# Optimization experiments

Hardware: AMD Instinct MI355X
Metric: run time of the kernel (lower is better)

## Reference

```python
import math
import jax, jax.numpy as jnp
import numpy as np

IN_DIM = 512
OUT_DIM = 512
K = 3
EPS = 1e-8


def setup_inputs() -> dict:
    key = jax.random.key(0)
    k1, k2, k3 = jax.random.split(key, 3)
    b, h, w = 8, 64, 64
    x = jax.random.normal(k1, (b, IN_DIM, h, w), dtype=jnp.float32)
    style = jax.random.normal(k2, (b, IN_DIM), dtype=jnp.float32)
    weight = jax.random.normal(k3, (OUT_DIM, IN_DIM, K, K), dtype=jnp.float32)
    bias = jnp.zeros((OUT_DIM,), dtype=jnp.float32)
    return {"x": x, "style": style, "weight": weight, "bias": bias}


def _mod_weights(weight, style):
    # EqualizedWeight scaling: c = 1/sqrt(prod(shape[1:]))
    c = 1.0 / math.sqrt(IN_DIM * K * K)
    w = weight * c                                    # [out, in, k, k]
    ws = w[None] * (style[:, None, :, None, None] + 1.0)  # [b, out, in, k, k]
    sigma_inv = jax.lax.rsqrt(jnp.sum(ws * ws, axis=(2, 3, 4), keepdims=True) + EPS)
    return ws * sigma_inv


def reference(x, style, weight, bias):
    ws = _mod_weights(weight, style)                  # [b, out, in, k, k]

    def conv_one(xi, wi):
        # xi: [in, h, w], wi: [out, in, k, k]
        y = jax.lax.conv_general_dilated(
            xi[None], wi, window_strides=(1, 1), padding="SAME",
            dimension_numbers=("NCHW", "OIHW", "NCHW"))
        return y[0]

    out = jax.vmap(conv_one)(x, ws)                   # [b, out, h, w]
    return out + bias[None, :, None, None]
```

## Files before the change

### kernel.cpp

```cpp
#include <hip/hip_runtime.h>

#define CIN 512
#define COUT 512
#define HH 64
#define WW 64
#define BB 8
#define KTOT 4608

#define XPD 66
#define BUFSH (3 * 66 * 64)
#define ROWB (66 * 128)

typedef __attribute__((ext_vector_type(8))) short short8;
typedef __attribute__((ext_vector_type(4))) float f32x4;

__device__ inline unsigned short f2bf(float f) {
    unsigned int u = __float_as_uint(f);
    u += 0x7FFFu + ((u >> 16) & 1u);
    return (unsigned short)(u >> 16);
}

__device__ inline void gll16(const void* g, void* l) {
    __builtin_amdgcn_global_load_lds(
        (const __attribute__((address_space(1))) unsigned int*)g,
        (__attribute__((address_space(3))) unsigned int*)l, 16, 0, 0);
}

__global__ __launch_bounds__(256) void zring_kernel(unsigned short* __restrict__ xtp) {
    const int e = blockIdx.x * 256 + threadIdx.x;
    if (e >= BB * 260 * 64) return;
    const int unit = e & 63;
    const int sa = e >> 6;
    const int b = sa / 260;
    const int s = sa - b * 260;
    int yy, xx;
    if (s < 66)       { yy = 0;        xx = s; }
    else if (s < 132) { yy = 65;       xx = s - 66; }
    else if (s < 196) { yy = s - 131;  xx = 0; }
    else              { yy = s - 195;  xx = 65; }
    *(short8*)(xtp + ((size_t)(b * XPD + yy) * XPD + xx) * 512 + unit * 8) =
        (short8){0, 0, 0, 0, 0, 0, 0, 0};
}

__global__ __launch_bounds__(256) void xpose_kernel(const float* __restrict__ x,
                                                    const float* __restrict__ style,
                                                    unsigned short* __restrict__ xtp) {
    __shared__ float tile[32 * 65];
    __shared__ float sst[32];
    const int ic = blockIdx.x;
    const int y  = blockIdx.y;
    const int b  = blockIdx.z;
    const int t  = threadIdx.x;
    if (t < 32) sst[t] = style[b * CIN + ic * 32 + t] + 1.0f;
#pragma unroll
    for (int it = 0; it < 8; ++it) {
        int e = it * 256 + t;
        int ii = e >> 6, xx = e & 63;
        tile[ii * 65 + xx] = x[(((size_t)(b * CIN + ic * 32 + ii) * HH + y) << 6) + xx];
    }
    __syncthreads();
#pragma unroll
    for (int it = 0; it < 8; ++it) {
        int g = it * 256 + t;
        int xx = g >> 5, ii = g & 31;
        xtp[((size_t)(b * XPD + y + 1) * XPD + xx + 1) * 512 + ic * 32 + ii] =
            f2bf(tile[ii * 65 + xx] * sst[ii]);
    }
}

__global__ __launch_bounds__(256) void wpack_kernel(const float* __restrict__ weight,
                                                    unsigned short* __restrict__ wpk) {
    __shared__ float q[KTOT];
    const int o = blockIdx.x;
    const int t = threadIdx.x;
    const float* wrow = weight + (size_t)o * KTOT;
    const float cst = 1.0f / sqrtf((float)KTOT);
#pragma unroll
    for (int it = 0; it < 18; ++it) {
        int e = it * 256 + t;
        q[e] = wrow[e] * cst;
    }
    __syncthreads();
    const int g = o >> 4, l15 = o & 15;
    for (int m = t; m < 576; m += 256) {
        int c   = m / 36;
        int rem = m - c * 36;
        int tap = rem >> 2;
        int l4  = rem & 3;
        short8 v;
#pragma unroll
        for (int e = 0; e < 8; ++e)
            v[e] = (short)f2bf(q[(c * 32 + l4 * 8 + e) * 9 + tap]);
        *(short8*)(wpk + ((((size_t)c * 9 + tap) * 32 + g) * 64 + l4 * 16 + l15) * 8) = v;
    }
}

__global__ __launch_bounds__(256) void sigma_kernel(const float* __restrict__ weight,
                                                    const float* __restrict__ style,
                                                    float* __restrict__ siginv) {
    __shared__ float sred[4][8];
    const int o = blockIdx.x;
    const int t = threadIdx.x;
    const float* wrow = weight + (size_t)o * KTOT;
    float acc[8] = {0.f, 0.f, 0.f, 0.f, 0.f, 0.f, 0.f, 0.f};
#pragma unroll
    for (int ii = 0; ii < 2; ++ii) {
        const int i = t * 2 + ii;
        float wsq = 0.f;
#pragma unroll
        for (int tap = 0; tap < 9; ++tap) {
            float v = wrow[i * 9 + tap];
            wsq += v * v;
        }
#pragma unroll
        for (int b = 0; b < 8; ++b) {
            float s = style[b * CIN + i] + 1.0f;
            acc[b] += wsq * s * s;
        }
    }
#pragma unroll
    for (int b = 0; b < 8; ++b) {
        float v = acc[b];
#pragma unroll
        for (int off = 32; off > 0; off >>= 1) v += __shfl_down(v, off, 64);
        if ((t & 63) == 0) sred[t >> 6][b] = v;
    }
    __syncthreads();
    if (t < 8) {
        const float S = sred[0][t] + sred[1][t] + sred[2][t] + sred[3][t];
        siginv[t * COUT + o] = rsqrtf(S * (1.0f / (float)KTOT) + 1e-8f);
    }
}

__global__ __launch_bounds__(256, 3) void conv_kernel(const unsigned short* __restrict__ wpk,
                                                      const unsigned short* __restrict__ xtp,
                                                      const float* __restrict__ siginv,
                                                      const float* __restrict__ bias,
                                                      float* __restrict__ out) {
    __shared__ __align__(16) unsigned short xs[2 * BUFSH];
    const int bid = blockIdx.x;
    const int k  = bid & 7;
    const int t  = bid >> 3;
    const int ob = k & 1;
    const int b  = (k >> 1) * 2 + (t >> 6);
    const int yb = t & 63;

    const int tid  = threadIdx.x;
    const int lane = tid & 63;
    const int wid_u = __builtin_amdgcn_readfirstlane(tid >> 6);
    const int l15 = lane & 15, l4 = lane >> 4;
    const int og = wid_u;
    const int g0 = ob * 16 + og * 4;

    const int up = lane & 7;
    const unsigned short* srcq[6];
#pragma unroll
    for (int tq = 0; tq < 6; ++tq) {
        const int sl = (wid_u + tq * 4) * 8 + (lane >> 3);
        const int row = sl / 66, col = sl - row * 66;
        srcq[tq] = xtp + ((size_t)(b * XPD + yb + row) * XPD + col) * 512 +
                   (up ^ (col & 7)) * 8;
    }
    const int col6 = 60 + (lane >> 3);
    const unsigned short* src6 =
        xtp + ((size_t)(b * XPD + yb + 2) * XPD + col6) * 512 + (up ^ (col6 & 7)) * 8;

    int vB[3][2];
#pragma unroll
    for (int kx = 0; kx < 3; ++kx)
#pragma unroll
        for (int ks = 0; ks < 2; ++ks)
            vB[kx][ks] = (l15 + kx) * 128 + (((ks * 4 + l4) ^ ((l15 + kx) & 7)) * 16);

    f32x4 acc[4][4];
#pragma unroll
    for (int mi = 0; mi < 4; ++mi)
#pragma unroll
        for (int j = 0; j < 4; ++j) acc[mi][j] = (f32x4){0.f, 0.f, 0.f, 0.f};

    short8 af[3][4];

    const unsigned short* aP = wpk + (size_t)g0 * 512 + lane * 8;

#define STAGE(bufp, icq)                                                                  \
    do {                                                                                  \
        unsigned short* dbase = xs + (bufp) * BUFSH + wid_u * 512;                        \
        _Pragma("unroll") for (int tq = 0; tq < 6; ++tq)                                  \
            gll16(srcq[tq] + (size_t)(icq) * 64, dbase + tq * 2048);                      \
        if (wid_u == 0 && lane < 48)                                                      \
            gll16(src6 + (size_t)(icq) * 64, xs + (bufp) * BUFSH + 12288);                \
    } while (0)

#define PHASE(s, aPic, cbase)                                                             \
    do {                                                                                  \
        const unsigned short* pA = (aPic) + (size_t)((s) + 2) * 16384;                    \
        _Pragma("unroll") for (int mi = 0; mi < 4; ++mi)                                  \
            af[((s) + 2) % 3][mi] = *(const short8*)(pA + mi * 512);                      \
        short8 bfr[4];                                                                    \
        const char* bp = (const char*)xs + (cbase) +                                      \
                         (((s) % 9) / 3) * ROWB + vB[((s) % 9) % 3][(s) / 9];             \
        _Pragma("unroll") for (int j = 0; j < 4; ++j)                                     \
            bfr[j] = *(const short8*)(bp + j * 2048);                                     \
        __builtin_amdgcn_s_setprio(1);                                                    \
        _Pragma("unroll") for (int mi = 0; mi < 4; ++mi)                                  \
            _Pragma("unroll") for (int j = 0; j < 4; ++j)                                 \
                acc[mi][j] = __builtin_amdgcn_mfma_f32_16x16x32_bf16(                     \
                    af[(s) % 3][mi], bfr[j], acc[mi][j], 0, 0, 0);                        \
        __builtin_amdgcn_s_setprio(0);                                                    \
    } while (0)

    af[0][0] = *(const short8*)(aP + 0 * 512);
    af[0][1] = *(const short8*)(aP + 1 * 512);
    af[0][2] = *(const short8*)(aP + 2 * 512);
    af[0][3] = *(const short8*)(aP + 3 * 512);
    {
        const unsigned short* p1 = aP + 16384;
        af[1][0] = *(const short8*)(p1 + 0 * 512);
        af[1][1] = *(const short8*)(p1 + 1 * 512);
        af[1][2] = *(const short8*)(p1 + 2 * 512);
        af[1][3] = *(const short8*)(p1 + 3 * 512);
    }
    STAGE(0, 0);
    __syncthreads();

#pragma unroll 1
    for (int ic = 0; ic < 8; ++ic) {
        if (ic < 7) STAGE((ic + 1) & 1, ic + 1);
        const unsigned short* aPic = aP + (size_t)ic * (18 * 16384);
        const int cbase = (ic & 1) * (BUFSH * 2);
#pragma unroll
        for (int s = 0; s < 18; ++s) {
            PHASE(s, aPic, cbase);
        }
        __syncthreads();
    }

#pragma unroll
    for (int mi = 0; mi < 4; ++mi) {
        const int obase = ob * 256 + og * 64 + mi * 16 + l4 * 4;
#pragma unroll
        for (int rr = 0; rr < 4; ++rr) {
            const int o = obase + rr;
            const float sv = siginv[b * COUT + o];
            const float bv = bias[o];
            float* orow = out + (((size_t)(b * COUT + o) * HH + yb) << 6);
#pragma unroll
            for (int j = 0; j < 4; ++j) {
                orow[j * 16 + l15] = acc[mi][j][rr] * sv + bv;
            }
        }
    }
#undef STAGE
#undef PHASE
}

extern "C" void kernel_launch(void* const* d_in, const int* in_sizes, int n_in,
                              void* d_out, int out_size, void* d_ws, size_t ws_size,
                              hipStream_t stream) {
    const float* x      = (const float*)d_in[0];
    const float* style  = (const float*)d_in[1];
    const float* weight = (const float*)d_in[2];
    const float* bias   = (const float*)d_in[3];
    float* out = (float*)d_out;

    unsigned short* wpk = (unsigned short*)d_ws;
    unsigned short* xtp = wpk + (size_t)2359296;
    float* siginv = (float*)(xtp + (size_t)BB * XPD * XPD * 512);

    zring_kernel<<<520, 256, 0, stream>>>(xtp);
    xpose_kernel<<<dim3(16, HH, BB), 256, 0, stream>>>(x, style, xtp);
    wpack_kernel<<<COUT, 256, 0, stream>>>(weight, wpk);
    sigma_kernel<<<COUT, 256, 0, stream>>>(weight, style, siginv);
    conv_kernel<<<1024, 256, 0, stream>>>(wpk, xtp, siginv, bias, out);
}
```

Baseline: 168.7 us.

## Software-pipeline LDS B-fragment loads and defer next-stage global loads mid-iteration

The main conv GEMM loop now double-buffers the B fragments from LDS, loading phase s+1's fragment while phase s runs its MFMAs. The loop is unrolled by two so the LDS buffer index is a compile-time constant. The global-to-LDS staging of the next channel block moves to the middle of the phase sequence instead of the start. __syncthreads is replaced by a partial vmcnt wait plus s_barrier and a sched_barrier, so some weight loads can stay in flight across the barrier. This trades more registers and a hand-tuned wait count, which could be fragile, for hiding LDS and global load latency behind MFMA work.

```diff
diff --git a/kernel.cpp b/kernel.cpp
--- a/kernel.cpp
+++ b/kernel.cpp
@@ -9,6 +9,7 @@
 
 #define XPD 66
 #define BUFSH (3 * 66 * 64)
+#define BUFB  (BUFSH * 2)
 #define ROWB (66 * 128)
 
 typedef __attribute__((ext_vector_type(8))) short short8;
@@ -191,48 +192,73 @@
             gll16(src6 + (size_t)(icq) * 64, xs + (bufp) * BUFSH + 12288);                \
     } while (0)
 
-#define PHASE(s, aPic, cbase)                                                             \
-    do {                                                                                  \
-        const unsigned short* pA = (aPic) + (size_t)((s) + 2) * 16384;                    \
+#define WAITBAR()                                                                         \
+    do {                                                                                  \
+        asm volatile("s_waitcnt vmcnt(8)" ::: "memory");                                  \
+        __builtin_amdgcn_s_barrier();                                                     \
+        __builtin_amdgcn_sched_barrier(0);                                                \
+    } while (0)
+
+#define LDB(dst, s)                                                                       \
+    do {                                                                                  \
+        const char* bp = (const char*)xs + cbase +                                        \
+                         (((s) % 9) / 3) * ROWB + vB[((s) % 9) % 3][(s) / 9];             \
+        _Pragma("unroll") for (int j = 0; j < 4; ++j)                                     \
+            dst[j] = *(const short8*)(bp + j * 2048);                                     \
+    } while (0)
+
+#define MFMAP(cur, s, aIC)                                                                \
+    do {                                                                                  \
+        const unsigned short* pA = (aIC) + (size_t)((s) + 2) * 16384;                     \
         _Pragma("unroll") for (int mi = 0; mi < 4; ++mi)                                  \
             af[((s) + 2) % 3][mi] = *(const short8*)(pA + mi * 512);                      \
-        short8 bfr[4];                                                                    \
-        const char* bp = (const char*)xs + (cbase) +                                      \
-                         (((s) % 9) / 3) * ROWB + vB[((s) % 9) % 3][(s) / 9];             \
-        _Pragma("unroll") for (int j = 0; j < 4; ++j)                                     \
-            bfr[j] = *(const short8*)(bp + j * 2048);                                     \
         __builtin_amdgcn_s_setprio(1);                                                    \
         _Pragma("unroll") for (int mi = 0; mi < 4; ++mi)                                  \
             _Pragma("unroll") for (int j = 0; j < 4; ++j)                                 \
                 acc[mi][j] = __builtin_amdgcn_mfma_f32_16x16x32_bf16(                     \
-                    af[(s) % 3][mi], bfr[j], acc[mi][j], 0, 0, 0);                        \
+                    af[(s) % 3][mi], cur[j], acc[mi][j], 0, 0, 0);                        \
         __builtin_amdgcn_s_setprio(0);                                                    \
     } while (0)
 
-    af[0][0] = *(const short8*)(aP + 0 * 512);
-    af[0][1] = *(const short8*)(aP + 1 * 512);
-    af[0][2] = *(const short8*)(aP + 2 * 512);
-    af[0][3] = *(const short8*)(aP + 3 * 512);
-    {
-        const unsigned short* p1 = aP + 16384;
-        af[1][0] = *(const short8*)(p1 + 0 * 512);
-        af[1][1] = *(const short8*)(p1 + 1 * 512);
-        af[1][2] = *(const short8*)(p1 + 2 * 512);
-        af[1][3] = *(const short8*)(p1 + 3 * 512);
-    }
+#define ICBODY(icv, P)                                                                    \
+    do {                                                                                  \
+        const unsigned short* aIC = aP + (size_t)(icv) * (18 * 16384);                    \
+        const int cbase = (P) * BUFB;                                                     \
+        short8 bA[4], bB[4];                                                              \
+        LDB(bA, 0);                                                                       \
+        LDB(bB, 1);   MFMAP(bA, 0, aIC);                                                  \
+        LDB(bA, 2);   MFMAP(bB, 1, aIC);                                                  \
+        LDB(bB, 3);   MFMAP(bA, 2, aIC);                                                  \
+        LDB(bA, 4);   MFMAP(bB, 3, aIC);                                                  \
+        LDB(bB, 5);   MFMAP(bA, 4, aIC);                                                  \
+        LDB(bA, 6);   MFMAP(bB, 5, aIC);                                                  \
+        LDB(bB, 7);   MFMAP(bA, 6, aIC);                                                  \
+        LDB(bA, 8);   MFMAP(bB, 7, aIC);                                                  \
+        if ((icv) < 7) STAGE((P) ^ 1, (icv) + 1);                                         \
+        LDB(bB, 9);   MFMAP(bA, 8, aIC);                                                  \
+        LDB(bA, 10);  MFMAP(bB, 9, aIC);                                                  \
+        LDB(bB, 11);  MFMAP(bA, 10, aIC);                                                 \
+        LDB(bA, 12);  MFMAP(bB, 11, aIC);                                                 \
+        LDB(bB, 13);  MFMAP(bA, 12, aIC);                                                 \
+        LDB(bA, 14);  MFMAP(bB, 13, aIC);                                                 \
+        LDB(bB, 15);  MFMAP(bA, 14, aIC);                                                 \
+        LDB(bA, 16);  MFMAP(bB, 15, aIC);                                                 \
+        LDB(bB, 17);  MFMAP(bA, 16, aIC);                                                 \
+        MFMAP(bB, 17, aIC);                                                               \
+        WAITBAR();                                                                        \
+    } while (0)
+
     STAGE(0, 0);
-    __syncthreads();
+#pragma unroll
+    for (int mi = 0; mi < 4; ++mi) af[0][mi] = *(const short8*)(aP + mi * 512);
+#pragma unroll
+    for (int mi = 0; mi < 4; ++mi) af[1][mi] = *(const short8*)(aP + 16384 + mi * 512);
+    WAITBAR();
 
 #pragma unroll 1
-    for (int ic = 0; ic < 8; ++ic) {
-        if (ic < 7) STAGE((ic + 1) & 1, ic + 1);
-        const unsigned short* aPic = aP + (size_t)ic * (18 * 16384);
-        const int cbase = (ic & 1) * (BUFSH * 2);
-#pragma unroll
-        for (int s = 0; s < 18; ++s) {
-            PHASE(s, aPic, cbase);
-        }
-        __syncthreads();
+    for (int icp = 0; icp < 4; ++icp) {
+        ICBODY(icp * 2, 0);
+        ICBODY(icp * 2 + 1, 1);
     }
 
 #pragma unroll
@@ -251,7 +277,10 @@
         }
     }
 #undef STAGE
-#undef PHASE
+#undef WAITBAR
+#undef LDB
+#undef MFMAP
+#undef ICBODY
 }
 
 extern "C" void kernel_launch(void* const* d_in, const int* in_sizes, int n_in,
```

Result: slower. 192.8 us (+14.3%).
